# Kernel optimization log

Hardware: AMD Instinct MI355X
Metric: run time of the kernel (lower is better)

The kernel has to match this reference:

```python
import jax, jax.numpy as jnp
import numpy as np
import math

H, W = 128, 128  # output_dim = (H, W)
B = 4096


def setup_inputs() -> dict:
    key = jax.random.key(0)
    moments = jax.random.normal(key, (B, 6), dtype=jnp.float32)
    return {"moments": moments}


def reference(moments):
    sx, sy = float(W - 1), float(H - 1)
    # grid: [[x, y] for x in range(W) for y in range(H)] -> shape [W*H, 2]
    gx, gy = jnp.meshgrid(jnp.arange(W, dtype=jnp.float32),
                          jnp.arange(H, dtype=jnp.float32), indexing="ij")
    grid = jnp.stack([gx.reshape(-1), gy.reshape(-1)], axis=-1)  # [G, 2]

    scale = jnp.array([sx / 2.0, sy / 2.0], dtype=jnp.float32)
    mu = jnp.tanh(moments[:, :2]) * scale + scale  # [B, 2]

    t = jnp.tanh(moments[:, 2:5])
    lo = jnp.array([0.03, -0.999, 0.03], dtype=jnp.float32)
    hi = jnp.array([1.0, 0.999, 1.0], dtype=jnp.float32)
    t = jnp.clip(t, lo, hi)
    a = t[:, 0] * 3.0 * sx                                   # cov[0,0]
    b = t[:, 1] * jnp.sqrt(t[:, 0] * t[:, 2] * 9.0 * sx * sy)  # cov[0,1]
    c = t[:, 2] * 3.0 * sy                                   # cov[1,1]

    det = a * c - b * b  # closed-form 2x2 determinant
    it = 10.0 * jax.nn.sigmoid(moments[:, 5])
    norm = it / jnp.sqrt(det * (2.0 * math.pi) ** 2)  # [B]

    d = grid[None, :, :] - mu[:, None, :]  # [B, G, 2]
    dx, dy = d[..., 0], d[..., 1]
    # closed-form quadratic form d^T Sigma^{-1} d for 2x2 symmetric Sigma
    q = (c[:, None] * dx * dx - 2.0 * b[:, None] * dx * dy + a[:, None] * dy * dy) / det[:, None]
    img = norm[:, None] * jnp.exp(-0.5 * q)  # [B, G]
    # reshape (B, W, H) then transpose -> (B, H, W), matching tf reference
    return jnp.transpose(img.reshape(-1, W, H), (0, 2, 1))
```

## Files before the change

kernel.cpp:

```cpp
#include <hip/hip_runtime.h>
#include <math.h>

#define HH 128
#define WW 128

__global__ __launch_bounds__(256) void MomentsToImage_kernel(
    const float* __restrict__ moments, float* __restrict__ out) {
    const int b = blockIdx.x;
    const float* m = moments + (size_t)b * 6;

    const float sx = (float)(WW - 1);
    const float sy = (float)(HH - 1);

    float m0 = m[0], m1 = m[1], m2 = m[2], m3 = m[3], m4 = m[4], m5 = m[5];

    float mux = tanhf(m0) * (sx * 0.5f) + (sx * 0.5f);
    float muy = tanhf(m1) * (sy * 0.5f) + (sy * 0.5f);

    float t0 = fminf(fmaxf(tanhf(m2), 0.03f),   1.0f);
    float t1 = fminf(fmaxf(tanhf(m3), -0.999f), 0.999f);
    float t2 = fminf(fmaxf(tanhf(m4), 0.03f),   1.0f);

    float a  = t0 * (3.0f * sx);
    float bb = t1 * sqrtf(t0 * t2 * (9.0f * sx * sy));
    float c  = t2 * (3.0f * sy);

    float det = a * c - bb * bb;
    float it  = 10.0f / (1.0f + __expf(-m5));
    float norm = it / (6.28318530717958647692f * sqrtf(det));

    float inv_det = 1.0f / det;
    float P = -0.5f * c * inv_det;
    float Q =  bb * inv_det;
    float R = -0.5f * a * inv_det;

    float4* out4 = (float4*)(out + (size_t)b * (HH * WW));

    #pragma unroll
    for (int i = 0; i < 16; ++i) {
        int v = i * 256 + threadIdx.x;
        int p = v << 2;
        float dy = (float)(p >> 7) - muy;
        float dx = (float)(p & 127) - mux;

        float rterm = R * dy * dy;
        float qdy   = Q * dy;

        float4 o;
        float d0 = dx;
        o.x = norm * __expf((P * d0 + qdy) * d0 + rterm);
        float d1 = dx + 1.0f;
        o.y = norm * __expf((P * d1 + qdy) * d1 + rterm);
        float d2 = dx + 2.0f;
        o.z = norm * __expf((P * d2 + qdy) * d2 + rterm);
        float d3 = dx + 3.0f;
        o.w = norm * __expf((P * d3 + qdy) * d3 + rterm);
        out4[v] = o;
    }
}

extern "C" void kernel_launch(void* const* d_in, const int* in_sizes, int n_in,
                              void* d_out, int out_size, void* d_ws, size_t ws_size,
                              hipStream_t stream) {
    const float* moments = (const float*)d_in[0];
    float* out = (float*)d_out;
    int B = in_sizes[0] / 6;
    MomentsToImage_kernel<<<dim3(B), dim3(256), 0, stream>>>(moments, out);
}
```

Baseline: 252.0 us.

## Precompute per-batch Gaussian constants in setup kernel, fold norm into exp2, nontemporal stores

Moves the per-image tanh/sqrt/sigmoid setup into a separate small kernel that writes eight constants per batch to workspace. The main kernel then folds the log2e scale and log(norm) into the exponent, so each pixel needs only a raw exp2 with no multiply. Output is written with nontemporal stores to avoid polluting the cache. The cost is an extra kernel launch and a workspace round trip, and using log/exp2 for the norm may change rounding slightly.

```diff
diff --git a/kernel.cpp b/kernel.cpp
--- a/kernel.cpp
+++ b/kernel.cpp
@@ -1,40 +1,54 @@
 #include <hip/hip_runtime.h>
-#include <math.h>
 
 #define HH 128
 #define WW 128
 
-__global__ __launch_bounds__(256) void MomentsToImage_kernel(
-    const float* __restrict__ moments, float* __restrict__ out) {
-    const int b = blockIdx.x;
+typedef float vfloat4 __attribute__((ext_vector_type(4)));
+
+
+__global__ __launch_bounds__(256) void setup_kernel(
+    const float* __restrict__ moments, float* __restrict__ cst, int B) {
+    int b = blockIdx.x * 256 + threadIdx.x;
+    if (b >= B) return;
     const float* m = moments + (size_t)b * 6;
 
     const float sx = (float)(WW - 1);
     const float sy = (float)(HH - 1);
+    const float L2E = 1.44269504088896340736f;
 
-    float m0 = m[0], m1 = m[1], m2 = m[2], m3 = m[3], m4 = m[4], m5 = m[5];
+    float mux = tanhf(m[0]) * (sx * 0.5f) + (sx * 0.5f);
+    float muy = tanhf(m[1]) * (sy * 0.5f) + (sy * 0.5f);
 
-    float mux = tanhf(m0) * (sx * 0.5f) + (sx * 0.5f);
-    float muy = tanhf(m1) * (sy * 0.5f) + (sy * 0.5f);
-
-    float t0 = fminf(fmaxf(tanhf(m2), 0.03f),   1.0f);
-    float t1 = fminf(fmaxf(tanhf(m3), -0.999f), 0.999f);
-    float t2 = fminf(fmaxf(tanhf(m4), 0.03f),   1.0f);
+    float t0 = fminf(fmaxf(tanhf(m[2]), 0.03f),   1.0f);
+    float t1 = fminf(fmaxf(tanhf(m[3]), -0.999f), 0.999f);
+    float t2 = fminf(fmaxf(tanhf(m[4]), 0.03f),   1.0f);
 
     float a  = t0 * (3.0f * sx);
     float bb = t1 * sqrtf(t0 * t2 * (9.0f * sx * sy));
     float c  = t2 * (3.0f * sy);
 
-    float det = a * c - bb * bb;
-    float it  = 10.0f / (1.0f + __expf(-m5));
+    float det  = a * c - bb * bb;
+    float it   = 10.0f / (1.0f + expf(-m[5]));
     float norm = it / (6.28318530717958647692f * sqrtf(det));
 
-    float inv_det = 1.0f / det;
-    float P = -0.5f * c * inv_det;
-    float Q =  bb * inv_det;
-    float R = -0.5f * a * inv_det;
+    float k = -0.5f * L2E / det;
+    vfloat4 c0 = {mux, muy, c * k, -2.0f * bb * k};
+    vfloat4 c1 = {a * k, __builtin_amdgcn_logf(norm), 0.0f, 0.0f};
 
-    float4* out4 = (float4*)(out + (size_t)b * (HH * WW));
+    vfloat4* o = (vfloat4*)(cst + (size_t)b * 8);
+    o[0] = c0;
+    o[1] = c1;
+}
+
+__global__ __launch_bounds__(256) void MomentsToImage_kernel(
+    const float* __restrict__ cst, float* __restrict__ out) {
+    const int b = blockIdx.x;
+    const float* s = cst + (size_t)b * 8;
+
+    float mux = s[0], muy = s[1];
+    float P2 = s[2], Q2 = s[3], R2 = s[4], C = s[5];
+
+    vfloat4* out4 = (vfloat4*)(out + (size_t)b * (HH * WW));
 
     #pragma unroll
     for (int i = 0; i < 16; ++i) {
@@ -43,19 +57,19 @@
         float dy = (float)(p >> 7) - muy;
         float dx = (float)(p & 127) - mux;
 
-        float rterm = R * dy * dy;
-        float qdy   = Q * dy;
+        float base = fmaf(R2 * dy, dy, C);
+        float qdy  = Q2 * dy;
 
-        float4 o;
+        vfloat4 o;
         float d0 = dx;
-        o.x = norm * __expf((P * d0 + qdy) * d0 + rterm);
+        o.x = __builtin_amdgcn_exp2f(fmaf(fmaf(P2, d0, qdy), d0, base));
         float d1 = dx + 1.0f;
-        o.y = norm * __expf((P * d1 + qdy) * d1 + rterm);
+        o.y = __builtin_amdgcn_exp2f(fmaf(fmaf(P2, d1, qdy), d1, base));
         float d2 = dx + 2.0f;
-        o.z = norm * __expf((P * d2 + qdy) * d2 + rterm);
+        o.z = __builtin_amdgcn_exp2f(fmaf(fmaf(P2, d2, qdy), d2, base));
         float d3 = dx + 3.0f;
-        o.w = norm * __expf((P * d3 + qdy) * d3 + rterm);
-        out4[v] = o;
+        o.w = __builtin_amdgcn_exp2f(fmaf(fmaf(P2, d3, qdy), d3, base));
+        __builtin_nontemporal_store(o, &out4[v]);
     }
 }
 
@@ -64,6 +78,9 @@
                               hipStream_t stream) {
     const float* moments = (const float*)d_in[0];
     float* out = (float*)d_out;
+    float* cst = (float*)d_ws;
     int B = in_sizes[0] / 6;
-    MomentsToImage_kernel<<<dim3(B), dim3(256), 0, stream>>>(moments, out);
+
+    setup_kernel<<<dim3((B + 255) / 256), dim3(256), 0, stream>>>(moments, cst, B);
+    MomentsToImage_kernel<<<dim3(B), dim3(256), 0, stream>>>(cst, out);
 }
```

New measurement: 269.6 us. 7.0% more time.
